# Kernel optimization log

Measured on AMD Instinct MI355X. Metric: run time of the kernel, lower is better.

## Reference

```python
import jax, jax.numpy as jnp
import numpy as np

D_MODEL = 1024
NUM_HEADS = 16
D_K = D_MODEL // NUM_HEADS
B, S = 4, 2048
NEG_INF = -1e9


def _linear_params(key, d_out, d_in):
    k1, k2 = jax.random.split(key)
    lim = 1.0 / np.sqrt(d_in)
    w = jax.random.uniform(k1, (d_out, d_in), jnp.float32, -lim, lim)
    b = jax.random.uniform(k2, (d_out,), jnp.float32, -lim, lim)
    return w, b


def setup_inputs() -> dict:
    key = jax.random.key(0)
    ks = jax.random.split(key, 16)
    query = jax.random.normal(ks[0], (B, S, D_MODEL), jnp.float32)
    kk = jax.random.normal(ks[1], (B, S, D_MODEL), jnp.float32)
    vv = jax.random.normal(ks[2], (B, S, D_MODEL), jnp.float32)
    # causal mask, broadcastable to [B,H,Sq,Sk]
    mask = jnp.tril(jnp.ones((S, S), jnp.int32))[None, None]
    wq1, bq1 = _linear_params(ks[3], D_MODEL, D_MODEL)
    wq2, bq2 = _linear_params(ks[4], D_MODEL, D_MODEL)
    wk1, bk1 = _linear_params(ks[5], D_MODEL, D_MODEL)
    wk2, bk2 = _linear_params(ks[6], D_MODEL, D_MODEL)
    wv1, bv1 = _linear_params(ks[7], D_MODEL, D_MODEL)
    wv2, bv2 = _linear_params(ks[8], D_MODEL, D_MODEL)
    wo, bo = _linear_params(ks[9], D_MODEL, D_MODEL)
    return dict(query=query, key=kk, value=vv, mask=mask,
                wq1=wq1, bq1=bq1, wq2=wq2, bq2=bq2,
                wk1=wk1, bk1=bk1, wk2=wk2, bk2=bk2,
                wv1=wv1, bv1=bv1, wv2=wv2, bv2=bv2,
                wo=wo, bo=bo)


def _swiglu_proj(x, w1, b1, w2, b2):
    # F.silu(w1(x)) * w2(x)
    return jax.nn.silu(x @ w1.T + b1) * (x @ w2.T + b2)


def _split_heads(x):
    b, s, _ = x.shape
    return x.reshape(b, s, NUM_HEADS, D_K).transpose(0, 2, 1, 3)  # [B,H,S,dk]


def reference(query, key, value, mask,
              wq1, bq1, wq2, bq2,
              wk1, bk1, wk2, bk2,
              wv1, bv1, wv2, bv2,
              wo, bo):
    q = _split_heads(_swiglu_proj(query, wq1, bq1, wq2, bq2))
    k = _split_heads(_swiglu_proj(key, wk1, bk1, wk2, bk2))
    v = _split_heads(_swiglu_proj(value, wv1, bv1, wv2, bv2))
    scores = jnp.einsum('bhqd,bhkd->bhqk', q, k) / np.sqrt(D_K).astype(np.float32)
    scores = jnp.where(mask == 0, jnp.float32(NEG_INF), scores)
    attn = jax.nn.softmax(scores, axis=-1)
    x = jnp.einsum('bhqk,bhkd->bhqd', attn, v)  # [B,H,S,dk]
    x = x.transpose(0, 2, 1, 3).reshape(query.shape[0], -1, NUM_HEADS * D_K)
    return x @ wo.T + bo
```

## Files before the change

kernel.cpp:

```cpp
#include <hip/hip_runtime.h>


typedef __bf16 bf16;
typedef bf16 bf16x8 __attribute__((ext_vector_type(8)));
typedef float f32x4 __attribute__((ext_vector_type(4)));
typedef unsigned short u16;
typedef unsigned int u32;
typedef u16 u16x8 __attribute__((ext_vector_type(8)));
typedef u16 u16x4 __attribute__((ext_vector_type(4)));

#define DEVI static __device__ __forceinline__

DEVI u16 f2b(float f) {
  union { float f; u32 u; } v; v.f = f;
  u32 r = v.u + 0x7FFFu + ((v.u >> 16) & 1u);
  return (u16)(r >> 16);
}
DEVI f32x4 mfma16(bf16x8 a, bf16x8 b, f32x4 c) {
  return __builtin_amdgcn_mfma_f32_16x16x32_bf16(a, b, c, 0, 0, 0);
}
DEVI void gload16(const void* g, void* l) {
  __builtin_amdgcn_global_load_lds(
      (const __attribute__((address_space(1))) void*)g,
      (__attribute__((address_space(3))) void*)l, 16, 0, 0);
}

struct P6 { const float* p[6]; };

__global__ void cvt_wpair(P6 in, u16* __restrict__ out) {
  const int pair = blockIdx.y;
  const float* w1 = in.p[2 * pair];
  const float* w2 = in.p[2 * pair + 1];
  u16* dst = out + (size_t)pair * 2097152;
  const int i = blockIdx.x * 256 + threadIdx.x;
  const int v = i >> 7;
  const int k0 = (i & 127) << 3;
  const int t7 = v & 127;
  const int g = (t7 >> 4) & 1;
  const int c = (v >> 7) * 64 + ((t7 >> 5) << 4) + (t7 & 15);
  const float* src = (g ? w2 : w1) + (size_t)c * 1024 + k0;
  const f32x4 a = *(const f32x4*)src;
  const f32x4 b = *(const f32x4*)(src + 4);
  u16x8 wv;
#pragma unroll
  for (int j = 0; j < 4; ++j) { wv[j] = f2b(a[j]); wv[4 + j] = f2b(b[j]); }
  *(u16x8*)(dst + (size_t)v * 1024 + k0) = wv;
}

__global__ void cvt_x(const float* __restrict__ src, u16* __restrict__ dst) {
  const int i = blockIdx.x * 256 + threadIdx.x;
  const f32x4 a = ((const f32x4*)src)[i * 2];
  const f32x4 b = ((const f32x4*)src)[i * 2 + 1];
  u16x8 w;
#pragma unroll
  for (int j = 0; j < 4; ++j) { w[j] = f2b(a[j]); w[4 + j] = f2b(b[j]); }
  ((u16x8*)dst)[i] = w;
}

template<int MODE>
__global__ __launch_bounds__(512, 2) void gemm256(
    const u16* __restrict__ Ap, const u16* __restrict__ Wp,
    const float* __restrict__ b1, const float* __restrict__ b2,
    void* __restrict__ outp, float scale)
{
  extern __shared__ char smem[];
  const int t = threadIdx.x;
  const int lane = t & 63, wid = t >> 6;
  const int lg = lane >> 4, lc = lane & 15;
  const int wr = (wid >> 1) * 64;
  const int wc = (wid & 1) * 64;
  constexpr int NXB = (MODE == 2) ? 8 : 16;
  const int flat = blockIdx.y * NXB + blockIdx.x;
  const int w8 = flat >> 3, xcd = flat & 7;
  const int m0 = (xcd * 4 + w8 / NXB) * 256;
  const int bx = w8 % NXB;
  const int K = 1024;
  const int srow = lane >> 3, scolb = (lane & 7) << 4;

  const f32x4 fz = {0.f, 0.f, 0.f, 0.f};
  f32x4 acc[4][4];
#pragma unroll
  for (int i = 0; i < 4; ++i)
#pragma unroll
    for (int j = 0; j < 4; ++j) acc[i][j] = fz;

  auto STAGE = [&](int buf, int kt) {
    const int k0 = kt << 6;
    char* As = smem + buf * 49152;
    char* Ws = As + 32768;
#pragma unroll
    for (int p = 0; p < 4; ++p) {
      const int rb = wid * 32 + p * 8;
      const int row = rb + srow;
      const int ce = (scolb ^ ((row & 7) << 4)) >> 1;
      gload16(Ap + (size_t)(m0 + row) * K + k0 + ce, As + rb * 128);
    }
#pragma unroll
    for (int p = 0; p < 2; ++p) {
      const int rb = wid * 16 + p * 8;
      const int row = rb + srow;
      const int ce = (scolb ^ ((row & 7) << 4)) >> 1;
      gload16(Wp + (size_t)(bx * 128 + row) * K + k0 + ce, Ws + rb * 128);
    }
  };

  STAGE(0, 0);
  __syncthreads();
  for (int kt = 0; kt < 16; ++kt) {
    const int cur = kt & 1;
    if (kt < 15) STAGE(cur ^ 1, kt + 1);
    const char* As = smem + cur * 49152;
    const char* Ws = As + 32768;
#pragma unroll
    for (int kh = 0; kh < 2; ++kh) {
      bf16x8 af[4], bfr[4];
#pragma unroll
      for (int mf = 0; mf < 4; ++mf) {
        const int r = wr + mf * 16 + lc;
        af[mf] = *(const bf16x8*)(As + r * 128 + ((kh * 64 + (lg << 4)) ^ ((r & 7) << 4)));
      }
#pragma unroll
      for (int nf = 0; nf < 4; ++nf) {
        const int v = wc + nf * 16 + lc;
        bfr[nf] = *(const bf16x8*)(Ws + v * 128 + ((kh * 64 + (lg << 4)) ^ ((v & 7) << 4)));
      }
#pragma unroll
      for (int mf = 0; mf < 4; ++mf)
#pragma unroll
        for (int nf = 0; nf < 4; ++nf)
          acc[mf][nf] = mfma16(af[mf], bfr[nf], acc[mf][nf]);
    }
    __syncthreads();
  }
  if constexpr (MODE == 2) {
    float* Co = (float*)outp;
#pragma unroll
    for (int mf = 0; mf < 4; ++mf)
#pragma unroll
      for (int nf = 0; nf < 4; ++nf) {
        const int r0 = m0 + wr + mf * 16 + (lg << 2);
        const int C = bx * 128 + wc + nf * 16 + lc;
        const float bv = b1[C];
#pragma unroll
        for (int j = 0; j < 4; ++j)
          Co[(size_t)(r0 + j) * 1024 + C] = acc[mf][nf][j] + bv;
      }
  } else {
    u16* Co = (u16*)outp;
#pragma unroll
    for (int mf = 0; mf < 4; ++mf) {
      const int r0 = m0 + wr + mf * 16 + (lg << 2);
#pragma unroll
      for (int p = 0; p < 2; ++p) {
        const int C = bx * 64 + (wid & 1) * 32 + p * 16 + lc;
        const float b1v = b1[C], b2v = b2[C];
        const int h = C >> 6, d = C & 63;
        if constexpr (MODE == 0) {
#pragma unroll
          for (int j = 0; j < 4; ++j) {
            const int r = r0 + j;
            const float x = acc[mf][2 * p][j] + b1v;
            const float y = acc[mf][2 * p + 1][j] + b2v;
            const float vv = (x / (1.f + __expf(-x))) * y * scale;
            const int bb = r >> 11, s = r & 2047;
            Co[((size_t)(bb * 16 + h) * 2048 + s) * 64 + d] = f2b(vv);
          }
        } else {
          u16x4 wv;
#pragma unroll
          for (int j = 0; j < 4; ++j) {
            const float x = acc[mf][2 * p][j] + b1v;
            const float y = acc[mf][2 * p + 1][j] + b2v;
            wv[j] = f2b((x / (1.f + __expf(-x))) * y);
          }
          const int bb = r0 >> 11, s0 = r0 & 2047;
          *(u16x4*)(Co + ((size_t)(bb * 16 + h) * 64 + d) * 2048 + s0) = wv;
        }
      }
    }
  }
}

__global__ __launch_bounds__(256, 4) void attn_fwd(
    const u16* __restrict__ Q, const u16* __restrict__ Kk,
    const u16* __restrict__ Vt, u16* __restrict__ O)
{
  __shared__ char smem[40960];
  char* Pw = smem + 32768 + (threadIdx.x >> 6) * 2048;
  const int t = threadIdx.x;
  const int lane = t & 63, wid = t >> 6;
  const int lg = lane >> 4, lc = lane & 15;
  const int flat = blockIdx.y * 16 + blockIdx.x;
  const int fl2 = (flat & 7) * 128 + (flat >> 3);
  const int qi = fl2 & 15;
  const int bh = fl2 >> 4;
  const int b = bh >> 4, h = bh & 15;
  const f32x4 fz = {0.f, 0.f, 0.f, 0.f};
  const float THR = 11.5f;

  bf16x8 onesb;
#pragma unroll
  for (int j = 0; j < 8; ++j) onesb[j] = (bf16)1.0f;

  auto STAGE = [&](int buf, int kt) {
    const int kbase = kt << 6;
    char* Kb = smem + buf * 16384;
    char* Vb = Kb + 8192;
#pragma unroll
    for (int p = 0; p < 4; ++p) {
      const int idx = wid * 4 + p;
      const int rb = (idx & 7) * 8;
      const int row = rb + (lane >> 3);
      const int ce = (((lane & 7) << 4) ^ ((row & 7) << 4)) >> 1;
      if (idx < 8)
        gload16(Kk + ((size_t)bh * 2048 + kbase + row) * 64 + ce, Kb + rb * 128);
      else
        gload16(Vt + ((size_t)bh * 64 + row) * 2048 + kbase + ce, Vb + rb * 128);
    }
  };

  for (int pass = 0; pass < 2; ++pass) {
    const int qc = pass ? (31 - qi) : qi;
    const int q0 = qc * 64;
    const int qw = q0 + wid * 16;

    bf16x8 qf[2];
#pragma unroll
    for (int kh = 0; kh < 2; ++kh) {
      const int r = qw + lc;
      qf[kh] = *(const bf16x8*)(Q + ((size_t)bh * 2048 + r) * 64 + kh * 32 + lg * 8);
    }

    f32x4 o[4], lacc = fz;
    float mrow[4];
#pragma unroll
    for (int dn = 0; dn < 4; ++dn) o[dn] = fz;
#pragma unroll
    for (int j = 0; j < 4; ++j) mrow[j] = -1e30f;

    const int nt = qc + 1;
    STAGE(0, 0);
    __syncthreads();
    for (int kt = 0; kt < nt; ++kt) {
      const int cur = kt & 1;
      if (kt + 1 < nt) STAGE(cur ^ 1, kt + 1);
      const int kbase = kt << 6;
      const char* Ks = smem + cur * 16384;
      const char* Vs = Ks + 8192;
      f32x4 sf[4];
#pragma unroll
      for (int nf = 0; nf < 4; ++nf) sf[nf] = fz;
      __builtin_amdgcn_s_setprio(1);
#pragma unroll
      for (int kh = 0; kh < 2; ++kh) {
        bf16x8 kb[4];
#pragma unroll
        for (int nf = 0; nf < 4; ++nf) {
          const int r = nf * 16 + lc;
          kb[nf] = *(const bf16x8*)(Ks + r * 128 + ((kh * 64 + (lg << 4)) ^ ((r & 7) << 4)));
        }
#pragma unroll
        for (int nf = 0; nf < 4; ++nf)
          sf[nf] = mfma16(qf[kh], kb[nf], sf[nf]);
      }
      __builtin_amdgcn_s_setprio(0);
      if (kbase + 63 > qw) {
#pragma unroll
        for (int nf = 0; nf < 4; ++nf)
#pragma unroll
          for (int j = 0; j < 4; ++j) {
            const int qr = qw + (lg << 2) + j;
            const int kc = kbase + nf * 16 + lc;
            if (kc > qr) sf[nf][j] = -1e30f;
          }
      }
      {
        float pm[4];
#pragma unroll
        for (int j = 0; j < 4; ++j)
          pm[j] = fmaxf(fmaxf(sf[0][j], sf[1][j]), fmaxf(sf[2][j], sf[3][j]));
        bool ok = true;
#pragma unroll
        for (int j = 0; j < 4; ++j) ok &= (pm[j] <= mrow[j] + THR);
        if (!__all(ok)) {
#pragma unroll
          for (int dd = 1; dd <= 8; dd <<= 1)
#pragma unroll
            for (int j = 0; j < 4; ++j)
              pm[j] = fmaxf(pm[j], __shfl_xor(pm[j], dd, 64));
          float scj[4];
#pragma unroll
          for (int j = 0; j < 4; ++j) {
            const float mn = fmaxf(mrow[j], pm[j]);
            scj[j] = exp2f(mrow[j] - mn);
            mrow[j] = mn;
          }
#pragma unroll
          for (int dn = 0; dn < 4; ++dn)
#pragma unroll
            for (int j = 0; j < 4; ++j)
              o[dn][j] *= scj[j];
#pragma unroll
          for (int j = 0; j < 4; ++j) lacc[j] *= scj[j];
        }
#pragma unroll
        for (int nf = 0; nf < 4; ++nf)
#pragma unroll
          for (int j = 0; j < 4; ++j) {
            const float p = exp2f(sf[nf][j] - mrow[j]);
            const int pr = (lg << 2) + j;
            const int pcb = (nf * 16 + lc) << 1;
            *(u16*)(Pw + pr * 128 + (pcb ^ ((pr & 7) << 4))) = f2b(p);
          }
      }
      __builtin_amdgcn_s_setprio(1);
#pragma unroll
      for (int kh = 0; kh < 2; ++kh) {
        const int pr = lc;
        const bf16x8 pa = *(const bf16x8*)(Pw + pr * 128 + ((kh * 64 + (lg << 4)) ^ ((pr & 7) << 4)));
        lacc = mfma16(pa, onesb, lacc);
#pragma unroll
        for (int dn = 0; dn < 4; ++dn) {
          const int vr = dn * 16 + lc;
          const bf16x8 vb = *(const bf16x8*)(Vs + vr * 128 + ((kh * 64 + (lg << 4)) ^ ((vr & 7) << 4)));
          o[dn] = mfma16(pa, vb, o[dn]);
        }
      }
      __builtin_amdgcn_s_setprio(0);
      __syncthreads();
    }
#pragma unroll
    for (int j = 0; j < 4; ++j) {
      const float inv = __builtin_amdgcn_rcpf(lacc[j]);
      const int s = qw + (lg << 2) + j;
#pragma unroll
      for (int dn = 0; dn < 4; ++dn) {
        const int d = dn * 16 + lc;
        O[((size_t)(b * 2048 + s) * 16 + h) * 64 + d] = f2b(o[dn][j] * inv);
      }
    }
  }
}

extern "C" void kernel_launch(void* const* d_in, const int* in_sizes, int n_in,
                              void* d_out, int out_size, void* d_ws, size_t ws_size,
                              hipStream_t stream)
{
  (void)in_sizes; (void)n_in; (void)out_size; (void)ws_size;
  const float* xq  = (const float*)d_in[0];
  const float* xk  = (const float*)d_in[1];
  const float* xv  = (const float*)d_in[2];
  const float* wq1 = (const float*)d_in[4];
  const float* bq1 = (const float*)d_in[5];
  const float* wq2 = (const float*)d_in[6];
  const float* bq2 = (const float*)d_in[7];
  const float* wk1 = (const float*)d_in[8];
  const float* bk1 = (const float*)d_in[9];
  const float* wk2 = (const float*)d_in[10];
  const float* bk2 = (const float*)d_in[11];
  const float* wv1 = (const float*)d_in[12];
  const float* bv1 = (const float*)d_in[13];
  const float* wv2 = (const float*)d_in[14];
  const float* bv2 = (const float*)d_in[15];
  const float* wo  = (const float*)d_in[16];
  const float* bo  = (const float*)d_in[17];

  char* ws = (char*)d_ws;
  u16* WB = (u16*)ws;
  u16* XB = (u16*)(ws + 14680064);
  u16* QB = (u16*)(ws + 48234496);
  u16* KB = (u16*)(ws + 65011712);
  u16* VT = (u16*)(ws + 81788928);
  u16* AO = XB;
  u16* WCQ = WB;
  u16* WCK = WB + 2097152;
  u16* WCV = WB + 4194304;
  u16* WO  = WB + 6291456;

  P6 p6 = {{wq1, wq2, wk1, wk2, wv1, wv2}};
  cvt_wpair<<<dim3(1024, 3), 256, 0, stream>>>(p6, WB);
  cvt_x<<<512, 256, 0, stream>>>(wo, WO);

  const float QSCALE = 0.125f * 1.44269504088896f;
  const dim3 gs(16, 32);
  cvt_x<<<4096, 256, 0, stream>>>(xq, XB);
  gemm256<0><<<gs, 512, 98304, stream>>>(XB, WCQ, bq1, bq2, QB, QSCALE);
  cvt_x<<<4096, 256, 0, stream>>>(xk, XB);
  gemm256<0><<<gs, 512, 98304, stream>>>(XB, WCK, bk1, bk2, KB, 1.0f);
  cvt_x<<<4096, 256, 0, stream>>>(xv, XB);
  gemm256<1><<<gs, 512, 98304, stream>>>(XB, WCV, bv1, bv2, VT, 1.0f);
  attn_fwd<<<dim3(16, 64), 256, 0, stream>>>(QB, KB, VT, AO);
  gemm256<2><<<dim3(8, 32), 512, 98304, stream>>>(AO, WO, bo, nullptr, d_out, 1.0f);
}
```

Baseline: 262.2 us.

## Keep attention P in registers via transposed MFMA and batch Q/K projections

The attention kernel now computes transposed scores (K·Q) so each lane owns a single query row. P is converted to bf16 with packed cvt and redistributed through permlane32 swaps and shuffles instead of a round trip through LDS. The row sum is accumulated in scalar registers instead of an extra MFMA against a ones vector, and the output is written with vectorized stores. Separately, the Q and K input conversions and projection GEMMs are merged into dual launches over separate workspace buffers, which cuts launch count and tail effects at the cost of more register shuffling and a more complex lane mapping.

```diff
diff --git a/kernel.cpp b/kernel.cpp
--- a/kernel.cpp
+++ b/kernel.cpp
@@ -23,6 +23,14 @@
   __builtin_amdgcn_global_load_lds(
       (const __attribute__((address_space(1))) void*)g,
       (__attribute__((address_space(3))) void*)l, 16, 0, 0);
+}
+DEVI u32 cvtpk(float lo, float hi) {
+  u32 r;
+  asm("v_cvt_pk_bf16_f32 %0, %1, %2" : "=v"(r) : "v"(lo), "v"(hi));
+  return r;
+}
+DEVI void pswap(u32& a, u32& b) {
+  asm("v_permlane32_swap_b32 %0, %1" : "+v"(a), "+v"(b));
 }
 
 struct P6 { const float* p[6]; };
@@ -47,7 +55,10 @@
   *(u16x8*)(dst + (size_t)v * 1024 + k0) = wv;
 }
 
-__global__ void cvt_x(const float* __restrict__ src, u16* __restrict__ dst) {
+__global__ void cvt_x(const float* __restrict__ s0, u16* __restrict__ d0,
+                      const float* __restrict__ s1, u16* __restrict__ d1) {
+  const float* src = blockIdx.y ? s1 : s0;
+  u16* dst = blockIdx.y ? d1 : d0;
   const int i = blockIdx.x * 256 + threadIdx.x;
   const f32x4 a = ((const f32x4*)src)[i * 2];
   const f32x4 b = ((const f32x4*)src)[i * 2 + 1];
@@ -57,21 +68,26 @@
   ((u16x8*)dst)[i] = w;
 }
 
-template<int MODE>
-__global__ __launch_bounds__(512, 2) void gemm256(
-    const u16* __restrict__ Ap, const u16* __restrict__ Wp,
-    const float* __restrict__ b1, const float* __restrict__ b2,
-    void* __restrict__ outp, float scale)
+struct GArgs {
+  const u16* A; const u16* W;
+  const float* b1; const float* b2;
+  void* out; float scale;
+};
+
+template<int MODE, bool DUAL>
+__global__ __launch_bounds__(512, 2) void gemm256(GArgs g0, GArgs g1)
 {
   extern __shared__ char smem[];
+  const int fl = blockIdx.x;
+  const GArgs g = (DUAL && fl >= 512) ? g1 : g0;
+  const int local = DUAL ? (fl & 511) : fl;
   const int t = threadIdx.x;
   const int lane = t & 63, wid = t >> 6;
   const int lg = lane >> 4, lc = lane & 15;
   const int wr = (wid >> 1) * 64;
   const int wc = (wid & 1) * 64;
   constexpr int NXB = (MODE == 2) ? 8 : 16;
-  const int flat = blockIdx.y * NXB + blockIdx.x;
-  const int w8 = flat >> 3, xcd = flat & 7;
+  const int xcd = local & 7, w8 = local >> 3;
   const int m0 = (xcd * 4 + w8 / NXB) * 256;
   const int bx = w8 % NXB;
   const int K = 1024;
@@ -93,14 +109,14 @@
       const int rb = wid * 32 + p * 8;
       const int row = rb + srow;
       const int ce = (scolb ^ ((row & 7) << 4)) >> 1;
-      gload16(Ap + (size_t)(m0 + row) * K + k0 + ce, As + rb * 128);
+      gload16(g.A + (size_t)(m0 + row) * K + k0 + ce, As + rb * 128);
     }
 #pragma unroll
     for (int p = 0; p < 2; ++p) {
       const int rb = wid * 16 + p * 8;
       const int row = rb + srow;
       const int ce = (scolb ^ ((row & 7) << 4)) >> 1;
-      gload16(Wp + (size_t)(bx * 128 + row) * K + k0 + ce, Ws + rb * 128);
+      gload16(g.W + (size_t)(bx * 128 + row) * K + k0 + ce, Ws + rb * 128);
     }
   };
 
@@ -133,27 +149,27 @@
     __syncthreads();
   }
   if constexpr (MODE == 2) {
-    float* Co = (float*)outp;
+    float* Co = (float*)g.out;
 #pragma unroll
     for (int mf = 0; mf < 4; ++mf)
 #pragma unroll
       for (int nf = 0; nf < 4; ++nf) {
         const int r0 = m0 + wr + mf * 16 + (lg << 2);
         const int C = bx * 128 + wc + nf * 16 + lc;
-        const float bv = b1[C];
+        const float bv = g.b1[C];
 #pragma unroll
         for (int j = 0; j < 4; ++j)
           Co[(size_t)(r0 + j) * 1024 + C] = acc[mf][nf][j] + bv;
       }
   } else {
-    u16* Co = (u16*)outp;
+    u16* Co = (u16*)g.out;
 #pragma unroll
     for (int mf = 0; mf < 4; ++mf) {
       const int r0 = m0 + wr + mf * 16 + (lg << 2);
 #pragma unroll
       for (int p = 0; p < 2; ++p) {
         const int C = bx * 64 + (wid & 1) * 32 + p * 16 + lc;
-        const float b1v = b1[C], b2v = b2[C];
+        const float b1v = g.b1[C], b2v = g.b2[C];
         const int h = C >> 6, d = C & 63;
         if constexpr (MODE == 0) {
 #pragma unroll
@@ -161,7 +177,7 @@
             const int r = r0 + j;
             const float x = acc[mf][2 * p][j] + b1v;
             const float y = acc[mf][2 * p + 1][j] + b2v;
-            const float vv = (x / (1.f + __expf(-x))) * y * scale;
+            const float vv = (x / (1.f + __expf(-x))) * y * g.scale;
             const int bb = r >> 11, s = r & 2047;
             Co[((size_t)(bb * 16 + h) * 2048 + s) * 64 + d] = f2b(vv);
           }
@@ -185,8 +201,7 @@
     const u16* __restrict__ Q, const u16* __restrict__ Kk,
     const u16* __restrict__ Vt, u16* __restrict__ O)
 {
-  __shared__ char smem[40960];
-  char* Pw = smem + 32768 + (threadIdx.x >> 6) * 2048;
+  __shared__ char smem[32768];
   const int t = threadIdx.x;
   const int lane = t & 63, wid = t >> 6;
   const int lg = lane >> 4, lc = lane & 15;
@@ -197,10 +212,7 @@
   const int b = bh >> 4, h = bh & 15;
   const f32x4 fz = {0.f, 0.f, 0.f, 0.f};
   const float THR = 11.5f;
-
-  bf16x8 onesb;
-#pragma unroll
-  for (int j = 0; j < 8; ++j) onesb[j] = (bf16)1.0f;
+  const bool ev = ((lg & 1) == 0);
 
   auto STAGE = [&](int buf, int kt) {
     const int kbase = kt << 6;
@@ -221,22 +233,17 @@
 
   for (int pass = 0; pass < 2; ++pass) {
     const int qc = pass ? (31 - qi) : qi;
-    const int q0 = qc * 64;
-    const int qw = q0 + wid * 16;
+    const int qw = qc * 64 + wid * 16;
 
     bf16x8 qf[2];
 #pragma unroll
-    for (int kh = 0; kh < 2; ++kh) {
-      const int r = qw + lc;
-      qf[kh] = *(const bf16x8*)(Q + ((size_t)bh * 2048 + r) * 64 + kh * 32 + lg * 8);
-    }
-
-    f32x4 o[4], lacc = fz;
-    float mrow[4];
+    for (int kh = 0; kh < 2; ++kh)
+      qf[kh] = *(const bf16x8*)(Q + ((size_t)bh * 2048 + qw + lc) * 64 + kh * 32 + lg * 8);
+
+    f32x4 o[4];
 #pragma unroll
     for (int dn = 0; dn < 4; ++dn) o[dn] = fz;
-#pragma unroll
-    for (int j = 0; j < 4; ++j) mrow[j] = -1e30f;
+    float mrow = -1e30f, lsum = 0.f;
 
     const int nt = qc + 1;
     STAGE(0, 0);
@@ -244,12 +251,11 @@
     for (int kt = 0; kt < nt; ++kt) {
       const int cur = kt & 1;
       if (kt + 1 < nt) STAGE(cur ^ 1, kt + 1);
-      const int kbase = kt << 6;
       const char* Ks = smem + cur * 16384;
       const char* Vs = Ks + 8192;
-      f32x4 sf[4];
-#pragma unroll
-      for (int nf = 0; nf < 4; ++nf) sf[nf] = fz;
+      f32x4 sfT[4];
+#pragma unroll
+      for (int nf = 0; nf < 4; ++nf) sfT[nf] = fz;
       __builtin_amdgcn_s_setprio(1);
 #pragma unroll
       for (int kh = 0; kh < 2; ++kh) {
@@ -261,83 +267,88 @@
         }
 #pragma unroll
         for (int nf = 0; nf < 4; ++nf)
-          sf[nf] = mfma16(qf[kh], kb[nf], sf[nf]);
+          sfT[nf] = mfma16(kb[nf], qf[kh], sfT[nf]);
       }
       __builtin_amdgcn_s_setprio(0);
-      if (kbase + 63 > qw) {
+      if (kt == nt - 1) {
+        const int kb0 = kt * 64 + (lg << 2);
+        const int qq = qw + lc;
 #pragma unroll
         for (int nf = 0; nf < 4; ++nf)
 #pragma unroll
-          for (int j = 0; j < 4; ++j) {
-            const int qr = qw + (lg << 2) + j;
-            const int kc = kbase + nf * 16 + lc;
-            if (kc > qr) sf[nf][j] = -1e30f;
-          }
-      }
-      {
-        float pm[4];
-#pragma unroll
-        for (int j = 0; j < 4; ++j)
-          pm[j] = fmaxf(fmaxf(sf[0][j], sf[1][j]), fmaxf(sf[2][j], sf[3][j]));
-        bool ok = true;
-#pragma unroll
-        for (int j = 0; j < 4; ++j) ok &= (pm[j] <= mrow[j] + THR);
-        if (!__all(ok)) {
-#pragma unroll
-          for (int dd = 1; dd <= 8; dd <<= 1)
-#pragma unroll
-            for (int j = 0; j < 4; ++j)
-              pm[j] = fmaxf(pm[j], __shfl_xor(pm[j], dd, 64));
-          float scj[4];
-#pragma unroll
-          for (int j = 0; j < 4; ++j) {
-            const float mn = fmaxf(mrow[j], pm[j]);
-            scj[j] = exp2f(mrow[j] - mn);
-            mrow[j] = mn;
-          }
-#pragma unroll
-          for (int dn = 0; dn < 4; ++dn)
-#pragma unroll
-            for (int j = 0; j < 4; ++j)
-              o[dn][j] *= scj[j];
-#pragma unroll
-          for (int j = 0; j < 4; ++j) lacc[j] *= scj[j];
+          for (int j = 0; j < 4; ++j)
+            if (kb0 + nf * 16 + j > qq) sfT[nf][j] = -1e30f;
+      }
+      float pm = sfT[0][0];
+#pragma unroll
+      for (int nf = 0; nf < 4; ++nf)
+#pragma unroll
+        for (int j = 0; j < 4; ++j) pm = fmaxf(pm, sfT[nf][j]);
+      pm = fmaxf(pm, __shfl_xor(pm, 16));
+      pm = fmaxf(pm, __shfl_xor(pm, 32));
+      if (!__all(pm <= mrow + THR)) {
+        const float mn = fmaxf(mrow, pm);
+        const float sc = exp2f(mrow - mn);
+        mrow = mn;
+        lsum *= sc;
+#pragma unroll
+        for (int dn = 0; dn < 4; ++dn)
+#pragma unroll
+          for (int j = 0; j < 4; ++j) o[dn][j] *= sc;
+      }
+      float p[4][4];
+#pragma unroll
+      for (int nf = 0; nf < 4; ++nf)
+#pragma unroll
+        for (int j = 0; j < 4; ++j) {
+          p[nf][j] = exp2f(sfT[nf][j] - mrow);
+          lsum += p[nf][j];
         }
-#pragma unroll
-        for (int nf = 0; nf < 4; ++nf)
-#pragma unroll
-          for (int j = 0; j < 4; ++j) {
-            const float p = exp2f(sf[nf][j] - mrow[j]);
-            const int pr = (lg << 2) + j;
-            const int pcb = (nf * 16 + lc) << 1;
-            *(u16*)(Pw + pr * 128 + (pcb ^ ((pr & 7) << 4))) = f2b(p);
-          }
+      u32 pw[2][4];
+#pragma unroll
+      for (int kh = 0; kh < 2; ++kh) {
+        u32 A0 = cvtpk(p[2 * kh][0], p[2 * kh][1]);
+        u32 A1 = cvtpk(p[2 * kh][2], p[2 * kh][3]);
+        u32 B0 = cvtpk(p[2 * kh + 1][0], p[2 * kh + 1][1]);
+        u32 B1 = cvtpk(p[2 * kh + 1][2], p[2 * kh + 1][3]);
+        pswap(A0, B0);
+        pswap(A1, B1);
+        const u32 P0s = __shfl_xor(A0, 16);
+        const u32 Q0s = __shfl_xor(B0, 16);
+        const u32 P1s = __shfl_xor(A1, 16);
+        const u32 Q1s = __shfl_xor(B1, 16);
+        pw[kh][0] = ev ? A0 : Q0s;
+        pw[kh][1] = ev ? A1 : Q1s;
+        pw[kh][2] = ev ? P0s : B0;
+        pw[kh][3] = ev ? P1s : B1;
       }
       __builtin_amdgcn_s_setprio(1);
 #pragma unroll
       for (int kh = 0; kh < 2; ++kh) {
-        const int pr = lc;
-        const bf16x8 pa = *(const bf16x8*)(Pw + pr * 128 + ((kh * 64 + (lg << 4)) ^ ((pr & 7) << 4)));
-        lacc = mfma16(pa, onesb, lacc);
+        union { u32 u[4]; bf16x8 v; } pc;
+#pragma unroll
+        for (int w = 0; w < 4; ++w) pc.u[w] = pw[kh][w];
+        const bf16x8 pa = pc.v;
 #pragma unroll
         for (int dn = 0; dn < 4; ++dn) {
           const int vr = dn * 16 + lc;
           const bf16x8 vb = *(const bf16x8*)(Vs + vr * 128 + ((kh * 64 + (lg << 4)) ^ ((vr & 7) << 4)));
-          o[dn] = mfma16(pa, vb, o[dn]);
+          o[dn] = mfma16(vb, pa, o[dn]);
         }
       }
       __builtin_amdgcn_s_setprio(0);
       __syncthreads();
     }
-#pragma unroll
-    for (int j = 0; j < 4; ++j) {
-      const float inv = __builtin_amdgcn_rcpf(lacc[j]);
-      const int s = qw + (lg << 2) + j;
-#pragma unroll
-      for (int dn = 0; dn < 4; ++dn) {
-        const int d = dn * 16 + lc;
-        O[((size_t)(b * 2048 + s) * 16 + h) * 64 + d] = f2b(o[dn][j] * inv);
-      }
+    lsum += __shfl_xor(lsum, 16);
+    lsum += __shfl_xor(lsum, 32);
+    const float inv = __builtin_amdgcn_rcpf(lsum);
+    const size_t ob = ((size_t)(b * 2048 + qw + lc) * 16 + h) * 64 + (lg << 2);
+#pragma unroll
+    for (int dn = 0; dn < 4; ++dn) {
+      u16x4 wv;
+#pragma unroll
+      for (int j = 0; j < 4; ++j) wv[j] = f2b(o[dn][j] * inv);
+      *(u16x4*)(O + ob + dn * 16) = wv;
     }
   }
 }
@@ -367,11 +378,13 @@
 
   char* ws = (char*)d_ws;
   u16* WB = (u16*)ws;
-  u16* XB = (u16*)(ws + 14680064);
+  u16* XQ = (u16*)(ws + 14680064);
+  u16* XK = (u16*)(ws + 31457280);
   u16* QB = (u16*)(ws + 48234496);
   u16* KB = (u16*)(ws + 65011712);
   u16* VT = (u16*)(ws + 81788928);
-  u16* AO = XB;
+  u16* XV = XQ;
+  u16* AO = XK;
   u16* WCQ = WB;
   u16* WCK = WB + 2097152;
   u16* WCV = WB + 4194304;
@@ -379,16 +392,20 @@
 
   P6 p6 = {{wq1, wq2, wk1, wk2, wv1, wv2}};
   cvt_wpair<<<dim3(1024, 3), 256, 0, stream>>>(p6, WB);
-  cvt_x<<<512, 256, 0, stream>>>(wo, WO);
+  cvt_x<<<dim3(512, 1), 256, 0, stream>>>(wo, WO, wo, WO);
+  cvt_x<<<dim3(4096, 2), 256, 0, stream>>>(xq, XQ, xk, XK);
 
   const float QSCALE = 0.125f * 1.44269504088896f;
-  const dim3 gs(16, 32);
-  cvt_x<<<4096, 256, 0, stream>>>(xq, XB);
-  gemm256<0><<<gs, 512, 98304, stream>>>(XB, WCQ, bq1, bq2, QB, QSCALE);
-  cvt_x<<<4096, 256, 0, stream>>>(xk, XB);
-  gemm256<0><<<gs, 512, 98304, stream>>>(XB, WCK, bk1, bk2, KB, 1.0f);
-  cvt_x<<<4096, 256, 0, stream>>>(xv, XB);
-  gemm256<1><<<gs, 512, 98304, stream>>>(XB, WCV, bv1, bv2, VT, 1.0f);
+  GArgs gq = {XQ, WCQ, bq1, bq2, QB, QSCALE};
+  GArgs gk = {XK, WCK, bk1, bk2, KB, 1.0f};
+  gemm256<0, true><<<1024, 512, 98304, stream>>>(gq, gk);
+
+  cvt_x<<<dim3(4096, 1), 256, 0, stream>>>(xv, XV, xv, XV);
+  GArgs gv = {XV, WCV, bv1, bv2, VT, 1.0f};
+  gemm256<1, false><<<512, 512, 98304, stream>>>(gv, gv);
+
   attn_fwd<<<dim3(16, 64), 256, 0, stream>>>(QB, KB, VT, AO);
-  gemm256<2><<<dim3(8, 32), 512, 98304, stream>>>(AO, WO, bo, nullptr, d_out, 1.0f);
-}
+
+  GArgs go = {AO, WO, bo, nullptr, d_out, 1.0f};
+  gemm256<2, false><<<256, 512, 98304, stream>>>(go, go);
+}
```

New measurement: 244.6 us. 6.7% less time.
